# Kernel optimization log

Measured on AMD Instinct MI355X. Metric: run time of the kernel, lower is better.

## Reference

```python
import jax, jax.numpy as jnp
import numpy as np

C = 256
RED = 2
C2 = C // RED


def setup_inputs() -> dict:
    key = jax.random.key(0)
    ks = jax.random.split(key, 6)
    B, H, W = 8, 64, 64
    x = jax.random.normal(ks[0], (B, C, H, W), dtype=jnp.float32)
    # 1x1 convs stored as [out_ch, in_ch] matrices
    W1 = jax.random.normal(ks[1], (C2, C), dtype=jnp.float32) * (1.0 / np.sqrt(C))
    b1 = jax.random.normal(ks[2], (C2,), dtype=jnp.float32) * 0.01
    W2 = jax.random.normal(ks[3], (C, C2), dtype=jnp.float32) * (1.0 / np.sqrt(C2))
    b2 = jax.random.normal(ks[4], (C,), dtype=jnp.float32) * 0.01
    # torch inits scale to zeros; use randn so the residual branch is active
    scale = jax.random.normal(ks[5], (1, C, 1, 1), dtype=jnp.float32)
    return {"x": x, "W1": W1, "b1": b1, "W2": W2, "b2": b2, "scale": scale}


def reference(x, W1, b1, W2, b2, scale):
    B, Cc, H, Wd = x.shape
    # conv1 (1x1): [B,C,H,W] -> [B,C2,H,W]
    y = jnp.einsum('bchw,oc->bohw', x, W1) + b1[None, :, None, None]
    # flatten spatial, move channels last: [B, N, C2]
    y = y.reshape(B, C2, H * Wd).transpose(0, 2, 1)
    # unscaled self-attention over N spatial positions
    att = jax.nn.softmax(jnp.einsum('bmc,bnc->bmn', y, y), axis=-1)  # [B,N,N]
    out = jnp.einsum('bmn,bnc->bmc', att, y)  # [B,N,C2]
    # faithful to torch: raw .view(B,-1,H,W) WITHOUT permuting back
    out = out.reshape(B, C2, H, Wd)
    # conv2 (1x1): [B,C2,H,W] -> [B,C,H,W]
    out = jnp.einsum('bchw,oc->bohw', out, W2) + b2[None, :, None, None]
    return out * scale + x
```

## Files before the change

### kernel.cpp

```cpp
#include <hip/hip_runtime.h>

#define B_  8
#define C_  256
#define C2_ 128
#define N_  4096
#define LOG2E 1.44269504088896f

typedef _Float16 f16;
typedef _Float16 f16x8 __attribute__((ext_vector_type(8)));
typedef float f32x4  __attribute__((ext_vector_type(4)));

static __device__ __forceinline__ unsigned pk2(float a, float b) {
  return __builtin_bit_cast(unsigned, __builtin_amdgcn_cvt_pkrtz(a, b));
}

__global__ __launch_bounds__(256)
void prep_kernel(const float* __restrict__ W1, const float* __restrict__ W2,
                 f16* __restrict__ w1h, f16* __restrict__ w2h)
{
  int i = blockIdx.x * 256 + threadIdx.x;
  w1h[i] = (f16)W1[i];
  w2h[i] = (f16)W2[i];
}

__global__ __launch_bounds__(256, 3)
void conv1_kernel(const float* __restrict__ x,
                  const f16* __restrict__ w1h,
                  const float* __restrict__ b1,
                  f16* __restrict__ Y, f16* __restrict__ Yt)
{
  __shared__ __align__(16) char smem[49152];
  float* Xr = (float*)smem;
  f16*   Ah = (f16*)(smem + 32768);
  f16*   T  = (f16*)smem;

  const int t = threadIdx.x;
  const int w = t >> 6, lane = t & 63, quad = lane >> 4, l16 = lane & 15;
  const int b = blockIdx.x, nt0 = blockIdx.y;

#pragma unroll
  for (int pass = 0; pass < 8; pass++) {
    int c  = (t >> 3) + pass * 32;
    int n4 = t & 7;
    float4 v = *(const float4*)(x + ((long)(b * C_ + c)) * N_ + nt0 * 32 + n4 * 4);
    *(float4*)(&Xr[c * 32 + (n4 ^ (c & 7)) * 4]) = v;
  }
  __syncthreads();
#pragma unroll
  for (int pass = 0; pass < 4; pass++) {
    int n  = t & 31;
    int kb = (t >> 5) + pass * 8;
    f16x8 vh;
#pragma unroll
    for (int jj = 0; jj < 8; jj++) {
      int cc = kb * 8 + jj;
      vh[jj] = (f16)Xr[cc * 32 + ((n >> 2) ^ (cc & 7)) * 4 + (n & 3)];
    }
    *(f16x8*)(&Ah[n * 256 + (kb ^ (n & 7)) * 8]) = vh;
  }
  __syncthreads();

  f16x8 bh[2][8];
#pragma unroll
  for (int nt = 0; nt < 2; nt++) {
    int c2 = w * 32 + nt * 16 + l16;
#pragma unroll
    for (int ks = 0; ks < 8; ks++)
      bh[nt][ks] = *(const f16x8*)(w1h + c2 * C_ + ks * 32 + quad * 8);
  }

  f32x4 acc[2][2];
#pragma unroll
  for (int i = 0; i < 2; i++)
#pragma unroll
    for (int j = 0; j < 2; j++) acc[i][j] = (f32x4){0.f, 0.f, 0.f, 0.f};

#pragma unroll
  for (int ks = 0; ks < 8; ks++)
#pragma unroll
    for (int mt = 0; mt < 2; mt++) {
      f16x8 ah = *(const f16x8*)(&Ah[(mt * 16 + l16) * 256 + (((ks * 4 + quad) ^ (l16 & 7))) * 8]);
#pragma unroll
      for (int nt = 0; nt < 2; nt++)
        acc[mt][nt] = __builtin_amdgcn_mfma_f32_16x16x32_f16(ah, bh[nt][ks], acc[mt][nt], 0, 0, 0);
    }
  __syncthreads();

#pragma unroll
  for (int nt = 0; nt < 2; nt++) {
    int c2 = w * 32 + nt * 16 + l16;
    float bv = b1[c2];
#pragma unroll
    for (int mt = 0; mt < 2; mt++)
#pragma unroll
      for (int rg = 0; rg < 4; rg++) {
        int n = mt * 16 + quad * 4 + rg;
        T[c2 * 40 + n] = (f16)(acc[mt][nt][rg] + bv);
      }
  }
  __syncthreads();
#pragma unroll
  for (int pass = 0; pass < 2; pass++) {
    int r  = (t >> 2) + pass * 64;
    int c8 = (t & 3) * 8;
    f16x8 v = *(const f16x8*)(&T[r * 40 + c8]);
    *(f16x8*)(Yt + ((long)(b * C2_ + r)) * N_ + nt0 * 32 + c8) = v;
  }
#pragma unroll
  for (int pass = 0; pass < 2; pass++) {
    int row = t & 31;
    int cg  = (t >> 5) + pass * 8;
    f16x8 v;
#pragma unroll
    for (int jj = 0; jj < 8; jj++) v[jj] = T[(cg * 8 + jj) * 40 + row];
    *(f16x8*)(Y + ((long)(b * N_ + nt0 * 32 + row)) * C2_ + cg * 8) = v;
  }
}

__global__ __launch_bounds__(256, 2)
void attn_kernel(const f16* __restrict__ Y, const f16* __restrict__ Yt,
                 f16* __restrict__ Op, float* __restrict__ ls)
{
  __shared__ f16 Ks[64 * 128];
  __shared__ f16 Vs[128 * 64];
  __shared__ float nsqf[128];

  const int t = threadIdx.x;
  const int w = t >> 6, lane = t & 63, quad = lane >> 4, l16 = lane & 15;
  const int b = blockIdx.x, qt = blockIdx.y, s = blockIdx.z;
  const int ns = gridDim.z;
  const f16* Yb  = Y  + (long)b * N_ * C2_;
  const f16* Ytb = Yt + (long)b * C2_ * N_;
  const int g0 = (s * 64) / ns;
  const int g1 = ((s + 1) * 64) / ns;

  f16x8 qf[2][4];
#pragma unroll
  for (int mt = 0; mt < 2; mt++)
#pragma unroll
    for (int ks = 0; ks < 4; ks++)
      qf[mt][ks] = *(const f16x8*)(Yb + (long)(qt * 128 + w * 32 + mt * 16 + l16) * C2_ + ks * 32 + quad * 8);

  {
    int r = t >> 1, half = t & 1;
    float ss = 0.f;
#pragma unroll
    for (int j = 0; j < 8; j++) {
      f16x8 v = *(const f16x8*)(Yb + (long)(qt * 128 + r) * C2_ + half * 64 + j * 8);
#pragma unroll
      for (int e = 0; e < 8; e++) { float f = (float)v[e]; ss = fmaf(f, f, ss); }
    }
    ss += __shfl_xor(ss, 1);
    if (!half) nsqf[r] = ss;
  }

  {
    const int kb0 = g0 * 64;
#pragma unroll
    for (int pass = 0; pass < 4; pass++) {
      int r = (t >> 4) + pass * 16;
      f16x8 kv = *(const f16x8*)(Yb + (long)(kb0 + r) * C2_ + (t & 15) * 8);
      *(f16x8*)(&Ks[r * 128 + (((t & 15)) ^ (r & 15)) * 8]) = kv;
    }
#pragma unroll
    for (int pass = 0; pass < 4; pass++) {
      int d = (t >> 3) + pass * 32;
      f16x8 vv = *(const f16x8*)(Ytb + (long)d * N_ + kb0 + (t & 7) * 8);
      *(f16x8*)(&Vs[d * 64 + (((t & 7)) ^ (d & 7)) * 8]) = vv;
    }
  }
  __syncthreads();

  float nm[2];
  nm[0] = nsqf[w * 32 + l16] * LOG2E;
  nm[1] = nsqf[w * 32 + 16 + l16] * LOG2E;

  f16x8 ones8;
#pragma unroll
  for (int j = 0; j < 8; j++) ones8[j] = (f16)1.0f;

  f32x4 Oa[2][8];
#pragma unroll
  for (int i = 0; i < 2; i++)
#pragma unroll
    for (int j = 0; j < 8; j++) Oa[i][j] = (f32x4){0.f, 0.f, 0.f, 0.f};
  f32x4 lac[2] = {(f32x4){0.f,0.f,0.f,0.f}, (f32x4){0.f,0.f,0.f,0.f}};

#pragma unroll 1
  for (int g = g0; g < g1; g++) {
    f16x8 stK[4], stV[4];
    if (g + 1 < g1) {
      int nb = (g + 1) * 64;
#pragma unroll
      for (int pass = 0; pass < 4; pass++)
        stK[pass] = *(const f16x8*)(Yb + (long)(nb + (t >> 4) + pass * 16) * C2_ + (t & 15) * 8);
#pragma unroll
      for (int pass = 0; pass < 4; pass++)
        stV[pass] = *(const f16x8*)(Ytb + (long)((t >> 3) + pass * 32) * N_ + nb + (t & 7) * 8);
    }

    f32x4 S[4][2];
#pragma unroll
    for (int i = 0; i < 4; i++)
#pragma unroll
      for (int j = 0; j < 2; j++) S[i][j] = (f32x4){0.f, 0.f, 0.f, 0.f};
#pragma unroll
    for (int ks = 0; ks < 4; ks++) {
      f16x8 bfr[4];
#pragma unroll
      for (int nt = 0; nt < 4; nt++)
        bfr[nt] = *(const f16x8*)(&Ks[(nt * 16 + l16) * 128 + (((ks * 4 + quad) ^ l16)) * 8]);
#pragma unroll
      for (int nt = 0; nt < 4; nt++)
#pragma unroll
        for (int mt = 0; mt < 2; mt++)
          S[nt][mt] = __builtin_amdgcn_mfma_f32_16x16x32_f16(bfr[nt], qf[mt][ks], S[nt][mt], 0, 0, 0);
    }

    unsigned Xp[2][4][2];
#pragma unroll
    for (int mt = 0; mt < 2; mt++)
#pragma unroll
      for (int nt = 0; nt < 4; nt++) {
        float p0 = exp2f(fminf(fmaf(S[nt][mt][0], LOG2E, -nm[mt]), 11.0f));
        float p1 = exp2f(fminf(fmaf(S[nt][mt][1], LOG2E, -nm[mt]), 11.0f));
        float p2 = exp2f(fminf(fmaf(S[nt][mt][2], LOG2E, -nm[mt]), 11.0f));
        float p3 = exp2f(fminf(fmaf(S[nt][mt][3], LOG2E, -nm[mt]), 11.0f));
        Xp[mt][nt][0] = pk2(p0, p1);
        Xp[mt][nt][1] = pk2(p2, p3);
      }

    f16x8 pa[2][2];
    {
      const bool par = (quad & 1) != 0;
#pragma unroll
      for (int mt = 0; mt < 2; mt++) {
#pragma unroll
        for (int pr = 0; pr < 2; pr++)
#pragma unroll
          for (int d = 0; d < 2; d++) {
            auto r = __builtin_amdgcn_permlane32_swap(Xp[mt][2 * pr][d], Xp[mt][2 * pr + 1][d], false, false);
            Xp[mt][2 * pr][d]     = r[0];
            Xp[mt][2 * pr + 1][d] = r[1];
          }
#pragma unroll
        for (int ks2 = 0; ks2 < 2; ks2++) {
          unsigned lo0 = Xp[mt][2 * ks2][0],     lo1 = Xp[mt][2 * ks2][1];
          unsigned hi0 = Xp[mt][2 * ks2 + 1][0], hi1 = Xp[mt][2 * ks2 + 1][1];
          unsigned lo0x = (unsigned)__builtin_amdgcn_ds_swizzle((int)lo0, 0x401F);
          unsigned lo1x = (unsigned)__builtin_amdgcn_ds_swizzle((int)lo1, 0x401F);
          unsigned hi0x = (unsigned)__builtin_amdgcn_ds_swizzle((int)hi0, 0x401F);
          unsigned hi1x = (unsigned)__builtin_amdgcn_ds_swizzle((int)hi1, 0x401F);
          union { unsigned u[4]; f16x8 v; } P;
          P.u[0] = par ? hi0x : lo0;
          P.u[1] = par ? hi1x : lo1;
          P.u[2] = par ? hi0  : lo0x;
          P.u[3] = par ? hi1  : lo1x;
          pa[ks2][mt] = P.v;
        }
      }
    }

#pragma unroll
    for (int ks2 = 0; ks2 < 2; ks2++) {
      f16x8 vb[8];
#pragma unroll
      for (int dt = 0; dt < 8; dt++)
        vb[dt] = *(const f16x8*)(&Vs[(dt * 16 + l16) * 64 + (((ks2 * 4 + quad) ^ (l16 & 7))) * 8]);
#pragma unroll
      for (int mt = 0; mt < 2; mt++) {
#pragma unroll
        for (int dt = 0; dt < 8; dt++)
          Oa[mt][dt] = __builtin_amdgcn_mfma_f32_16x16x32_f16(pa[ks2][mt], vb[dt], Oa[mt][dt], 0, 0, 0);
        lac[mt] = __builtin_amdgcn_mfma_f32_16x16x32_f16(pa[ks2][mt], ones8, lac[mt], 0, 0, 0);
      }
    }

    __syncthreads();
    if (g + 1 < g1) {
#pragma unroll
      for (int pass = 0; pass < 4; pass++) {
        int r = (t >> 4) + pass * 16;
        *(f16x8*)(&Ks[r * 128 + (((t & 15)) ^ (r & 15)) * 8]) = stK[pass];
      }
#pragma unroll
      for (int pass = 0; pass < 4; pass++) {
        int d = (t >> 3) + pass * 32;
        *(f16x8*)(&Vs[d * 64 + (((t & 7)) ^ (d & 7)) * 8]) = stV[pass];
      }
    }
    __syncthreads();
  }

  const long rbase = ((long)s * B_ + b) * N_ + qt * 128;
#pragma unroll
  for (int mt = 0; mt < 2; mt++)
#pragma unroll
    for (int rg = 0; rg < 4; rg++) {
      int r = w * 32 + mt * 16 + quad * 4 + rg;
#pragma unroll
      for (int dt = 0; dt < 8; dt++)
        Op[(rbase + r) * C2_ + dt * 16 + l16] = (f16)Oa[mt][dt][rg];
      if (l16 == 0) ls[rbase + r] = lac[mt][rg];
    }
}

__global__ __launch_bounds__(256, 4)
void conv2_kernel(const f16* __restrict__ Op, const float* __restrict__ ls,
                  const f16* __restrict__ w2h,
                  const float* __restrict__ b2,
                  const float* __restrict__ scale,
                  const float* __restrict__ x,
                  float* __restrict__ out, int ns)
{
  __shared__ f16 Or[128 * 72];
  __shared__ f16 Bsw[64 * 128];
  __shared__ float invL[128];

  const int t = threadIdx.x;
  const int w = t >> 6, lane = t & 63, quad = lane >> 4, l16 = lane & 15;
  const int b = blockIdx.x, pt = blockIdx.y, oh = blockIdx.z;
  const long base0 = (long)b * 524288;

  if (t < 128) {
    int q = t * 32 + (pt >> 1);
    float l = 0.f;
    for (int si = 0; si < ns; si++)
      l += ls[(long)si * 32768 + (long)b * N_ + q];
    invL[t] = 1.0f / fmaxf(l, 1e-20f);
  }
  __syncthreads();

#pragma unroll
  for (int pass = 0; pass < 4; pass++) {
    int j = (t >> 3) + pass * 32;
    int c8 = (t & 7) * 8;
    float fa[8] = {0.f,0.f,0.f,0.f,0.f,0.f,0.f,0.f};
    for (int si = 0; si < ns; si++) {
      f16x8 a = *(const f16x8*)(Op + (long)si * 4194304 + base0 + (long)j * N_ + pt * 64 + c8);
#pragma unroll
      for (int jj = 0; jj < 8; jj++) fa[jj] += (float)a[jj];
    }
    float iv = invL[j];
    f16x8 r;
#pragma unroll
    for (int jj = 0; jj < 8; jj++)
      r[jj] = (f16)(fa[jj] * iv);
    *(f16x8*)(&Or[j * 72 + c8]) = r;
  }
  __syncthreads();
#pragma unroll
  for (int pass = 0; pass < 4; pass++) {
    int p = t & 63;
    int q = (t >> 6) + pass * 4;
    f16x8 vv;
#pragma unroll
    for (int jj = 0; jj < 8; jj++) vv[jj] = Or[(q * 8 + jj) * 72 + p];
    *(f16x8*)(&Bsw[p * 128 + ((q ^ (p & 15))) * 8]) = vv;
  }
  __syncthreads();

  f32x4 acc[2][4];
#pragma unroll
  for (int i = 0; i < 2; i++)
#pragma unroll
    for (int j = 0; j < 4; j++) acc[i][j] = (f32x4){0.f, 0.f, 0.f, 0.f};

#pragma unroll
  for (int ks = 0; ks < 4; ks++) {
    f16x8 bfr[4];
#pragma unroll
    for (int nt = 0; nt < 4; nt++)
      bfr[nt] = *(const f16x8*)(&Bsw[(nt * 16 + l16) * 128 + (((ks * 4 + quad) ^ l16)) * 8]);
#pragma unroll
    for (int mt = 0; mt < 2; mt++) {
      int o = oh * 128 + w * 32 + mt * 16 + l16;
      f16x8 ah = *(const f16x8*)(w2h + o * C2_ + ks * 32 + quad * 8);
#pragma unroll
      for (int nt = 0; nt < 4; nt++)
        acc[mt][nt] = __builtin_amdgcn_mfma_f32_16x16x32_f16(ah, bfr[nt], acc[mt][nt], 0, 0, 0);
    }
  }
#pragma unroll
  for (int mt = 0; mt < 2; mt++)
#pragma unroll
    for (int rg = 0; rg < 4; rg++) {
      int o = oh * 128 + w * 32 + mt * 16 + quad * 4 + rg;
      float so = scale[o], bo = b2[o];
#pragma unroll
      for (int nt = 0; nt < 4; nt++) {
        int p = pt * 64 + nt * 16 + l16;
        long xo = ((long)b * C_ + o) * N_ + p;
        out[xo] = (acc[mt][nt][rg] + bo) * so + x[xo];
      }
    }
}

extern "C" void kernel_launch(void* const* d_in, const int* in_sizes, int n_in,
                              void* d_out, int out_size, void* d_ws, size_t ws_size,
                              hipStream_t stream) {
  const float* x     = (const float*)d_in[0];
  const float* W1    = (const float*)d_in[1];
  const float* b1    = (const float*)d_in[2];
  const float* W2    = (const float*)d_in[3];
  const float* b2    = (const float*)d_in[4];
  const float* scale = (const float*)d_in[5];
  float* outp = (float*)d_out;

  const size_t NE = (size_t)B_ * N_ * C2_;

  int ns = 4;
  while (ns > 2) {
    size_t need = (size_t)(2 + ns) * NE * 2 + (size_t)ns * (B_ * N_ * 4) + 131072;
    if (need <= ws_size) break;
    ns--;
  }

  f16* Y   = (f16*)d_ws;
  f16* Yt  = Y + NE;
  f16* Op  = Yt + NE;
  float* ls = (float*)(Op + (size_t)ns * NE);
  f16* w1h = (f16*)(ls + (size_t)ns * 32768);
  f16* w2h = w1h + 32768;

  prep_kernel <<<dim3(128),       dim3(256), 0, stream>>>(W1, W2, w1h, w2h);
  conv1_kernel<<<dim3(8, 128),    dim3(256), 0, stream>>>(x, w1h, b1, Y, Yt);
  attn_kernel <<<dim3(8, 32, ns), dim3(256), 0, stream>>>(Y, Yt, Op, ls);
  conv2_kernel<<<dim3(8, 64, 2),  dim3(256), 0, stream>>>(Op, ls, w2h, b2, scale, x, outp, ns);
}
```

Before: 217.8 us.

## Double-buffer K/V shared tiles in attention and fix key split to two

The attention kernel now holds two LDS buffers for K and V. Each iteration writes the prefetched next tile into the spare buffer, so one barrier per iteration replaces two. Swizzled LDS addresses are precomputed as per-thread base pointers to cut index arithmetic in the inner loop. The key-split count is fixed at 2 instead of choosing up to 4 from workspace size, which halves the grid and the partial-output traffic into conv2 but lowers parallelism. Doubling LDS to about 64KB per block may limit how many blocks fit per CU.

Measured after the change: 212.0 us. -2.7%, faster.

```diff
diff --git a/kernel.cpp b/kernel.cpp
--- a/kernel.cpp
+++ b/kernel.cpp
@@ -121,8 +121,8 @@
 void attn_kernel(const f16* __restrict__ Y, const f16* __restrict__ Yt,
                  f16* __restrict__ Op, float* __restrict__ ls)
 {
-  __shared__ f16 Ks[64 * 128];
-  __shared__ f16 Vs[128 * 64];
+  __shared__ f16 Ks[2][64 * 128];
+  __shared__ f16 Vs[2][128 * 64];
   __shared__ float nsqf[128];
 
   const int t = threadIdx.x;
@@ -134,6 +134,18 @@
   const int g0 = (s * 64) / ns;
   const int g1 = ((s + 1) * 64) / ns;
 
+  const int l3 = l16 & 3, l12 = l16 & 12, l4v = l16 & 4;
+  const f16* kp[4];
+#pragma unroll
+  for (int ks = 0; ks < 4; ks++)
+    kp[ks] = &Ks[0][l16 * 128 + (((ks * 4) ^ l12) + (quad ^ l3)) * 8];
+  const f16* vp[2];
+#pragma unroll
+  for (int ks2 = 0; ks2 < 2; ks2++)
+    vp[ks2] = &Vs[0][l16 * 64 + (((ks2 * 4) ^ l4v) + (quad ^ l3)) * 8];
+  f16* kwp = &Ks[0][(t >> 4) * 128 + ((t & 15) ^ (t >> 4)) * 8];
+  f16* vwp = &Vs[0][(t >> 3) * 64 + ((t & 7) ^ ((t >> 3) & 7)) * 8];
+
   f16x8 qf[2][4];
 #pragma unroll
   for (int mt = 0; mt < 2; mt++)
@@ -158,15 +170,13 @@
     const int kb0 = g0 * 64;
 #pragma unroll
     for (int pass = 0; pass < 4; pass++) {
-      int r = (t >> 4) + pass * 16;
-      f16x8 kv = *(const f16x8*)(Yb + (long)(kb0 + r) * C2_ + (t & 15) * 8);
-      *(f16x8*)(&Ks[r * 128 + (((t & 15)) ^ (r & 15)) * 8]) = kv;
+      f16x8 kv = *(const f16x8*)(Yb + (long)(kb0 + (t >> 4) + pass * 16) * C2_ + (t & 15) * 8);
+      *(f16x8*)(kwp + pass * 2048) = kv;
     }
 #pragma unroll
     for (int pass = 0; pass < 4; pass++) {
-      int d = (t >> 3) + pass * 32;
-      f16x8 vv = *(const f16x8*)(Ytb + (long)d * N_ + kb0 + (t & 7) * 8);
-      *(f16x8*)(&Vs[d * 64 + (((t & 7)) ^ (d & 7)) * 8]) = vv;
+      f16x8 vv = *(const f16x8*)(Ytb + (long)((t >> 3) + pass * 32) * N_ + kb0 + (t & 7) * 8);
+      *(f16x8*)(vwp + pass * 2048) = vv;
     }
   }
   __syncthreads();
@@ -186,10 +196,12 @@
     for (int j = 0; j < 8; j++) Oa[i][j] = (f32x4){0.f, 0.f, 0.f, 0.f};
   f32x4 lac[2] = {(f32x4){0.f,0.f,0.f,0.f}, (f32x4){0.f,0.f,0.f,0.f}};
 
+  int cur = 0;
 #pragma unroll 1
   for (int g = g0; g < g1; g++) {
     f16x8 stK[4], stV[4];
-    if (g + 1 < g1) {
+    const bool pf = (g + 1 < g1);
+    if (pf) {
       int nb = (g + 1) * 64;
 #pragma unroll
       for (int pass = 0; pass < 4; pass++)
@@ -198,6 +210,7 @@
       for (int pass = 0; pass < 4; pass++)
         stV[pass] = *(const f16x8*)(Ytb + (long)((t >> 3) + pass * 32) * N_ + nb + (t & 7) * 8);
     }
+    const int co = cur * 8192;
 
     f32x4 S[4][2];
 #pragma unroll
@@ -209,7 +222,7 @@
       f16x8 bfr[4];
 #pragma unroll
       for (int nt = 0; nt < 4; nt++)
-        bfr[nt] = *(const f16x8*)(&Ks[(nt * 16 + l16) * 128 + (((ks * 4 + quad) ^ l16)) * 8]);
+        bfr[nt] = *(const f16x8*)(kp[ks] + co + nt * 2048);
 #pragma unroll
       for (int nt = 0; nt < 4; nt++)
 #pragma unroll
@@ -266,7 +279,7 @@
       f16x8 vb[8];
 #pragma unroll
       for (int dt = 0; dt < 8; dt++)
-        vb[dt] = *(const f16x8*)(&Vs[(dt * 16 + l16) * 64 + (((ks2 * 4 + quad) ^ (l16 & 7))) * 8]);
+        vb[dt] = *(const f16x8*)(vp[ks2] + co + dt * 1024);
 #pragma unroll
       for (int mt = 0; mt < 2; mt++) {
 #pragma unroll
@@ -276,20 +289,17 @@
       }
     }
 
-    __syncthreads();
-    if (g + 1 < g1) {
-#pragma unroll
-      for (int pass = 0; pass < 4; pass++) {
-        int r = (t >> 4) + pass * 16;
-        *(f16x8*)(&Ks[r * 128 + (((t & 15)) ^ (r & 15)) * 8]) = stK[pass];
-      }
-#pragma unroll
-      for (int pass = 0; pass < 4; pass++) {
-        int d = (t >> 3) + pass * 32;
-        *(f16x8*)(&Vs[d * 64 + (((t & 7)) ^ (d & 7)) * 8]) = stV[pass];
-      }
-    }
-    __syncthreads();
+    if (pf) {
+      const int no = (cur ^ 1) * 8192;
+#pragma unroll
+      for (int pass = 0; pass < 4; pass++)
+        *(f16x8*)(kwp + no + pass * 2048) = stK[pass];
+#pragma unroll
+      for (int pass = 0; pass < 4; pass++)
+        *(f16x8*)(vwp + no + pass * 2048) = stV[pass];
+      cur ^= 1;
+      __syncthreads();
+    }
   }
 
   const long rbase = ((long)s * B_ + b) * N_ + qt * 128;
@@ -408,13 +418,7 @@
   float* outp = (float*)d_out;
 
   const size_t NE = (size_t)B_ * N_ * C2_;
-
-  int ns = 4;
-  while (ns > 2) {
-    size_t need = (size_t)(2 + ns) * NE * 2 + (size_t)ns * (B_ * N_ * 4) + 131072;
-    if (need <= ws_size) break;
-    ns--;
-  }
+  const int ns = 2;
 
   f16* Y   = (f16*)d_ws;
   f16* Yt  = Y + NE;
```
